# Optimization experiments

Hardware: AMD Instinct MI355X
Metric: run time of the kernel (lower is better)

Reference implementation:

```python
import jax, jax.numpy as jnp
import numpy as np

B, N = 1, 512
CS, CZ, H, CH, PQ, PV = 384, 128, 12, 16, 4, 8
INF, EPS = 1e5, 1e-8
SOFTPLUS_INV_1 = 0.541324854612918


def _init_linear(key, fan_in, fan_out):
    kw, kb = jax.random.split(key)
    std = float(1.0 / np.sqrt(fan_in))
    w = jax.random.normal(kw, (fan_in, fan_out), dtype=jnp.float32) * std
    b = jnp.zeros((fan_out,), dtype=jnp.float32)
    return w, b


def setup_inputs() -> dict:
    key = jax.random.key(0)
    ks = jax.random.split(key, 12)
    s = jax.random.normal(ks[0], (B, N, CS), dtype=jnp.float32)
    z = jax.random.normal(ks[1], (B, N, N, CZ), dtype=jnp.float32) * 0.1
    # proper rotation matrices via QR of random Gaussians
    rot, _ = jnp.linalg.qr(jax.random.normal(ks[2], (B, N, 3, 3), dtype=jnp.float32))
    trans = jax.random.normal(ks[3], (B, N, 3), dtype=jnp.float32) * 10.0
    mask = jnp.ones((B, N), dtype=jnp.float32)
    w_q, b_q = _init_linear(ks[4], CS, H * CH)
    w_kv, b_kv = _init_linear(ks[5], CS, 2 * H * CH)
    w_qp, b_qp = _init_linear(ks[6], CS, H * PQ * 3)
    w_kvp, b_kvp = _init_linear(ks[7], CS, H * (PQ + PV) * 3)
    w_b, b_b = _init_linear(ks[8], CZ, H)
    head_weights = jnp.full((H,), SOFTPLUS_INV_1, dtype=jnp.float32)
    concat_dim = H * (CZ + CH + PV * 4)
    # 'final' init -> zeros
    w_out = jnp.zeros((concat_dim, CS), dtype=jnp.float32)
    b_out = jnp.zeros((CS,), dtype=jnp.float32)
    return dict(s=s, z=z, rot=rot, trans=trans, mask=mask,
                w_q=w_q, b_q=b_q, w_kv=w_kv, b_kv=b_kv,
                w_qp=w_qp, b_qp=b_qp, w_kvp=w_kvp, b_kvp=b_kvp,
                w_b=w_b, b_b=b_b, head_weights=head_weights,
                w_out=w_out, b_out=b_out)


def reference(s, z, rot, trans, mask,
              w_q, b_q, w_kv, b_kv, w_qp, b_qp, w_kvp, b_kvp,
              w_b, b_b, head_weights, w_out, b_out):
    # scalar q/k/v: [B,N,H,CH]
    q = (s @ w_q + b_q).reshape(B, N, H, CH)
    kv = (s @ w_kv + b_kv).reshape(B, N, H, 2 * CH)
    k, v = kv[..., :CH], kv[..., CH:]

    def make_points(w, b, P):
        p = s @ w + b                                   # [B,N,3*H*P] (x|y|z chunks)
        p = jnp.moveaxis(p.reshape(B, N, 3, H * P), -2, -1)  # [B,N,H*P,3]
        p = jnp.einsum('bnij,bnpj->bnpi', rot, p) + trans[:, :, None]  # global frame
        return p.reshape(B, N, H, P, 3)

    q_pts = make_points(w_qp, b_qp, PQ)                 # [B,N,H,PQ,3]
    kv_pts = make_points(w_kvp, b_kvp, PQ + PV)
    k_pts, v_pts = kv_pts[..., :PQ, :], kv_pts[..., PQ:, :]

    # scalar QK attention + pair bias
    a = jnp.einsum('bqhc,bkhc->bhqk', q, k) * float(np.sqrt(1.0 / (3 * CH)))
    b_bias = z @ w_b + b_b                              # [B,N,N,H]
    a = a + float(np.sqrt(1.0 / 3.0)) * jnp.moveaxis(b_bias, -1, -3)

    # squared point-distance attention
    d = q_pts[:, :, None] - k_pts[:, None]              # [B,N,N,H,PQ,3]
    pt_att = jnp.sum(d * d, axis=-1)                    # [B,N,N,H,PQ]
    hw = jax.nn.softplus(head_weights) * float(np.sqrt(1.0 / (3 * (PQ * 9.0 / 2))))
    pt_att = -0.5 * jnp.sum(pt_att * hw[None, None, None, :, None], axis=-1)  # [B,N,N,H]
    a = a + jnp.moveaxis(pt_att, -1, -3)                # [B,H,N,N]

    sq_mask = (mask[:, :, None] * mask[:, None, :] - 1.0) * INF
    a = jax.nn.softmax(a + sq_mask[:, None], axis=-1)   # [B,H,N,N]

    # standard value path
    o = jnp.einsum('bhqk,bkhc->bqhc', a, v).reshape(B, N, H * CH)
    # point value path, rotated back to local frame
    o_pt = jnp.einsum('bhqk,bkhpc->bqhpc', a, v_pts)    # [B,N,H,PV,3]
    o_pt = jnp.einsum('bnji,bnhpj->bnhpi', rot, o_pt - trans[:, :, None, None])
    o_pt_norm = jnp.sqrt(jnp.sum(o_pt ** 2, axis=-1) + EPS).reshape(B, N, H * PV)
    o_pt = o_pt.reshape(B, N, H * PV, 3)
    # pair-weighted path
    o_pair = jnp.einsum('bhqk,bqkc->bqhc', a, z).reshape(B, N, H * CZ)

    o_cat = jnp.concatenate(
        [o, o_pt[..., 0], o_pt[..., 1], o_pt[..., 2], o_pt_norm, o_pair], axis=-1)
    return o_cat @ w_out + b_out
```

## Files before the change

### kernel.cpp

```cpp
#include <hip/hip_runtime.h>
#include <math.h>

#define NRES 512
#define CSD  384
#define CZD  128

#define OFF_Q     0
#define OFF_KT    98304
#define OFF_VC    196608
#define OFF_QP    458752
#define OFF_KPT   532480
#define OFF_A     606208
#define OFF_OCAT  3751936
#define OFF_WCAT  4833280
#define OFF_BCAT  (OFF_WCAT + 442368)
#define OFF_PRAWQ 5276800
#define OFF_PRAWK 5350528
#define OFF_PART  OFF_A

__global__ __launch_bounds__(256) void k_wcat(
    const float* __restrict__ w_q, const float* __restrict__ b_q,
    const float* __restrict__ w_kv, const float* __restrict__ b_kv,
    const float* __restrict__ w_qp, const float* __restrict__ b_qp,
    const float* __restrict__ w_kvp, const float* __restrict__ b_kvp,
    float* __restrict__ wcat, float* __restrict__ bcat)
{
    const int idx = blockIdx.x * 256 + threadIdx.x;
    if (idx < 442368) {
        const int k = idx / 1152, c = idx % 1152;
        float v;
        if (c < 192)      v = w_q[k*192 + c];
        else if (c < 576) v = w_kv[k*384 + (c - 192)];
        else if (c < 720) v = w_qp[k*144 + (c - 576)];
        else              v = w_kvp[k*432 + (c - 720)];
        wcat[idx] = v;
    } else if (idx < 443520) {
        const int c = idx - 442368;
        float v;
        if (c < 192)      v = b_q[c];
        else if (c < 576) v = b_kv[c - 192];
        else if (c < 720) v = b_qp[c - 576];
        else              v = b_kvp[c - 720];
        bcat[c] = v;
    }
}

__global__ __launch_bounds__(256) void k_proj2(
    const float* __restrict__ s, const float* __restrict__ wcat, const float* __restrict__ bcat,
    float* __restrict__ q, float* __restrict__ kkT, float* __restrict__ vcomb,
    float* __restrict__ praw_q, float* __restrict__ praw_kv)
{
    const int ct = blockIdx.x;
    const int n0 = blockIdx.y * 32;
    const int t = threadIdx.x;

    __shared__ float sT[32][34];
    __shared__ float wt[32][36];

    const int lr = t >> 3, lc4 = t & 7;
    const int tr = t >> 4, tc = t & 15;
    float4 sv4, wv4;

    sv4 = *(const float4*)&s[(n0 + lr) * CSD + lc4 * 4];
    wv4 = *(const float4*)&wcat[lr * 1152 + ct * 32 + lc4 * 4];
    sT[lc4*4+0][lr] = sv4.x; sT[lc4*4+1][lr] = sv4.y; sT[lc4*4+2][lr] = sv4.z; sT[lc4*4+3][lr] = sv4.w;
    *(float4*)&wt[lr][lc4*4] = wv4;
    __syncthreads();

    float a00 = 0.f, a01 = 0.f, a10 = 0.f, a11 = 0.f;

    for (int it = 0; it < 12; ++it) {
        if (it < 11) {
            const int k0 = (it + 1) * 32;
            sv4 = *(const float4*)&s[(n0 + lr) * CSD + k0 + lc4 * 4];
            wv4 = *(const float4*)&wcat[(k0 + lr) * 1152 + ct * 32 + lc4 * 4];
        }
        #pragma unroll
        for (int kx = 0; kx < 32; ++kx) {
            float2 ss = *(const float2*)&sT[kx][tr * 2];
            float2 ww = *(const float2*)&wt[kx][tc * 2];
            a00 += ss.x * ww.x; a01 += ss.x * ww.y;
            a10 += ss.y * ww.x; a11 += ss.y * ww.y;
        }
        __syncthreads();
        if (it < 11) {
            sT[lc4*4+0][lr] = sv4.x; sT[lc4*4+1][lr] = sv4.y; sT[lc4*4+2][lr] = sv4.z; sT[lc4*4+3][lr] = sv4.w;
            *(float4*)&wt[lr][lc4*4] = wv4;
            __syncthreads();
        }
    }

    float accv[2][2] = {{a00, a01}, {a10, a11}};
    #pragma unroll
    for (int i = 0; i < 2; ++i) {
        const int n = n0 + tr * 2 + i;
        #pragma unroll
        for (int j = 0; j < 2; ++j) {
            const int gcol = ct * 32 + tc * 2 + j;
            const float v = accv[i][j] + bcat[gcol];
            if (gcol < 192) {
                q[n*192 + gcol] = v;
            } else if (gcol < 576) {
                int g = gcol - 192, h = g >> 5, cc = g & 31;
                if (cc < 16) kkT[(h*16 + cc)*NRES + n] = v;
                else         vcomb[n*NRES + h*16 + (cc-16)] = v;
            } else if (gcol < 720) {
                praw_q[n*144 + (gcol - 576)] = v;
            } else {
                praw_kv[n*432 + (gcol - 720)] = v;
            }
        }
    }
}

__global__ __launch_bounds__(256) void k_rot(
    const float* __restrict__ praw_q, const float* __restrict__ praw_kv,
    const float* __restrict__ rot, const float* __restrict__ trans,
    float* __restrict__ q_pts, float* __restrict__ kptsT, float* __restrict__ vcomb)
{
    const int idx = blockIdx.x * 256 + threadIdx.x;
    const int n = idx / 192, u = idx % 192;
    const float* R = rot + n*9;
    const float* T = trans + n*3;
    float px, py, pz;
    if (u < 48) {
        px = praw_q[n*144 + u]; py = praw_q[n*144 + 48 + u]; pz = praw_q[n*144 + 96 + u];
    } else {
        int pt = u - 48;
        px = praw_kv[n*432 + pt]; py = praw_kv[n*432 + 144 + pt]; pz = praw_kv[n*432 + 288 + pt];
    }
    float x  = R[0]*px + R[1]*py + R[2]*pz + T[0];
    float y  = R[3]*px + R[4]*py + R[5]*pz + T[1];
    float zc = R[6]*px + R[7]*py + R[8]*pz + T[2];
    if (u < 48) {
        int o = (n*48 + u)*3;
        q_pts[o] = x; q_pts[o+1] = y; q_pts[o+2] = zc;
    } else {
        int pt = u - 48;
        int h = pt / 12, pp = pt % 12;
        if (pp < 4) {
            int dim = (h*4 + pp)*3;
            kptsT[(dim+0)*NRES + n] = x;
            kptsT[(dim+1)*NRES + n] = y;
            kptsT[(dim+2)*NRES + n] = zc;
        } else {
            int u2 = (h*8 + (pp-4))*3;
            vcomb[n*NRES + 192 + u2+0] = x;
            vcomb[n*NRES + 192 + u2+1] = y;
            vcomb[n*NRES + 192 + u2+2] = zc;
        }
    }
}

__global__ __launch_bounds__(256) void k_bias2(
    const float* __restrict__ z, const float* __restrict__ w_b, const float* __restrict__ b_b,
    float* __restrict__ biasT)
{
    const int qn = blockIdx.y;
    const int k0 = blockIdx.x * 64;
    const int t = threadIdx.x;
    __shared__ float zt[64*129];
    __shared__ float wb[1536];

    for (int i = t; i < 1536; i += 256) wb[i] = w_b[i];
    const float4* zp4 = (const float4*)(z + ((size_t)qn*NRES + k0)*CZD);
    #pragma unroll
    for (int r = 0; r < 8; ++r) {
        int idx = t + r*256;
        int kx = idx >> 5, c4 = idx & 31;
        float4 v4 = zp4[idx];
        float* dst = &zt[kx*129 + c4*4];
        dst[0] = v4.x; dst[1] = v4.y; dst[2] = v4.z; dst[3] = v4.w;
    }
    __syncthreads();

    const int k = t & 63;
    const int h0 = (t >> 6) * 3;
    float acc0 = b_b[h0], acc1 = b_b[h0+1], acc2 = b_b[h0+2];
    const float* zrow = &zt[k*129];
    #pragma unroll 4
    for (int c = 0; c < 128; ++c) {
        float zv = zrow[c];
        const float* wp = &wb[c*12 + h0];
        acc0 += zv * wp[0];
        acc1 += zv * wp[1];
        acc2 += zv * wp[2];
    }
    const size_t base = (size_t)qn*NRES + k0 + k;
    biasT[(size_t)(h0+0)*NRES*NRES + base] = acc0;
    biasT[(size_t)(h0+1)*NRES*NRES + base] = acc1;
    biasT[(size_t)(h0+2)*NRES*NRES + base] = acc2;
}

__global__ __launch_bounds__(256, 3) void k_row4(
    const float* __restrict__ z, const float* __restrict__ biasT,
    const float* __restrict__ q, const float* __restrict__ kkT, const float* __restrict__ vcomb,
    const float* __restrict__ q_pts, const float* __restrict__ kptsT,
    const float* __restrict__ head_weights, const float* __restrict__ mask,
    const float* __restrict__ rot, const float* __restrict__ trans,
    float* __restrict__ o_cat)
{
    const int qn = blockIdx.x;
    const int t = threadIdx.x;

    __shared__ float a_lds[12][521];
    __shared__ float pred[4][12][128];
    __shared__ float q_lds[192];
    __shared__ float qp_lds[144];
    __shared__ float hw_lds[12];
    __shared__ float optraw[288];

    if (t < 192) q_lds[t] = q[qn*192 + t];
    if (t < 144) qp_lds[t] = q_pts[qn*144 + t];
    if (t < 12)  hw_lds[t] = logf(1.f + expf(head_weights[t])) * 0.13608276f;
    __syncthreads();

    const float mq = mask[qn];
    for (int h = 0; h < 12; ++h) {
        float qv[16], qpv[12];
        #pragma unroll
        for (int c = 0; c < 16; ++c) qv[c] = q_lds[h*16+c];
        #pragma unroll
        for (int d = 0; d < 12; ++d) qpv[d] = qp_lds[h*12+d];
        const float hw = hw_lds[h];
        const float* kT  = kkT + h*16*NRES;
        const float* kpT = kptsT + h*12*NRES;
        const float* brow = biasT + (size_t)h*NRES*NRES + (size_t)qn*NRES;
        #pragma unroll
        for (int r = 0; r < 2; ++r) {
            const int kn = t + r*256;
            float acc = 0.f;
            #pragma unroll
            for (int c = 0; c < 16; ++c) acc += qv[c] * kT[c*NRES + kn];
            acc *= 0.14433757f;
            acc += 0.57735027f * brow[kn];
            float dsum = 0.f;
            #pragma unroll
            for (int d = 0; d < 12; ++d) { float df = qpv[d] - kpT[d*NRES + kn]; dsum += df*df; }
            a_lds[h][kn] = acc - 0.5f*hw*dsum + (mq*mask[kn]-1.f)*100000.f;
        }
    }
    __syncthreads();

    {
        const int w = t >> 6, lane = t & 63;
        for (int h = w; h < 12; h += 4) {
            float m = -1e30f;
            #pragma unroll
            for (int i = 0; i < 8; ++i) m = fmaxf(m, a_lds[h][lane + i*64]);
            #pragma unroll
            for (int off = 32; off > 0; off >>= 1) m = fmaxf(m, __shfl_xor(m, off));
            float ss = 0.f;
            #pragma unroll
            for (int i = 0; i < 8; ++i) {
                float e = __expf(a_lds[h][lane + i*64] - m);
                a_lds[h][lane + i*64] = e;
                ss += e;
            }
            #pragma unroll
            for (int off = 32; off > 0; off >>= 1) ss += __shfl_xor(ss, off);
            float inv = 1.f / ss;
            #pragma unroll
            for (int i = 0; i < 8; ++i) a_lds[h][lane + i*64] *= inv;
        }
    }
    __syncthreads();

    {
        const int c4 = t & 31, kgrp = t >> 5;
        const float4* zp = (const float4*)(z + (size_t)qn*NRES*CZD) + c4;
        float4 acc4[12];
        #pragma unroll
        for (int h = 0; h < 12; ++h) acc4[h] = make_float4(0.f,0.f,0.f,0.f);

        #pragma unroll 8
        for (int kn = kgrp; kn < NRES; kn += 8) {
            float4 zv = zp[kn*32];
            #pragma unroll
            for (int h = 0; h < 12; ++h) {
                float av = a_lds[h][kn];
                acc4[h].x += av*zv.x; acc4[h].y += av*zv.y;
                acc4[h].z += av*zv.z; acc4[h].w += av*zv.w;
            }
        }
        #pragma unroll
        for (int h = 0; h < 12; ++h) {
            acc4[h].x += __shfl_xor(acc4[h].x, 32);
            acc4[h].y += __shfl_xor(acc4[h].y, 32);
            acc4[h].z += __shfl_xor(acc4[h].z, 32);
            acc4[h].w += __shfl_xor(acc4[h].w, 32);
        }
        const int wave = t >> 6;
        if ((t & 63) < 32) {
            #pragma unroll
            for (int h = 0; h < 12; ++h) {
                pred[wave][h][c4*4+0] = acc4[h].x;
                pred[wave][h][c4*4+1] = acc4[h].y;
                pred[wave][h][c4*4+2] = acc4[h].z;
                pred[wave][h][c4*4+3] = acc4[h].w;
            }
        }
        __syncthreads();
        for (int i = t; i < 1536; i += 256) {
            int h = i >> 7, c = i & 127;
            float v = pred[0][h][c] + pred[1][h][c] + pred[2][h][c] + pred[3][h][c];
            o_cat[qn*2112 + 576 + h*128 + c] = v;
        }
    }

    if (t < 240) {
        const int ch0 = 2*t, ch1 = 2*t + 1;
        const int hA = (ch0 < 192) ? (ch0 >> 4) : (ch0 - 192) / 24;
        const int hB = (ch1 < 192) ? (ch1 >> 4) : (ch1 - 192) / 24;
        float aAcc = 0.f, bAcc = 0.f;
        const float2* vp2 = (const float2*)vcomb + t;
        #pragma unroll 8
        for (int kn = 0; kn < NRES; ++kn) {
            float2 v = vp2[(size_t)kn*256];
            aAcc += a_lds[hA][kn] * v.x;
            bAcc += a_lds[hB][kn] * v.y;
        }
        if (ch0 < 192) o_cat[qn*2112 + ch0] = aAcc;
        else           optraw[ch0 - 192] = aAcc;
        if (ch1 < 192) o_cat[qn*2112 + ch1] = bAcc;
        else           optraw[ch1 - 192] = bAcc;
    }
    __syncthreads();

    if (t < 96) {
        const float* R = rot + qn*9;
        const float* T = trans + qn*3;
        float ox = optraw[t*3]   - T[0];
        float oy = optraw[t*3+1] - T[1];
        float oz = optraw[t*3+2] - T[2];
        float x  = R[0]*ox + R[3]*oy + R[6]*oz;
        float y  = R[1]*ox + R[4]*oy + R[7]*oz;
        float zc = R[2]*ox + R[5]*oy + R[8]*oz;
        float* ob = o_cat + qn*2112;
        ob[192 + t] = x;
        ob[288 + t] = y;
        ob[384 + t] = zc;
        ob[480 + t] = sqrtf(x*x + y*y + zc*zc + 1e-8f);
    }
}

__global__ __launch_bounds__(256) void k_out2(
    const float* __restrict__ o_cat, const float* __restrict__ w_out, float* __restrict__ part)
{
    const int ct = blockIdx.x;
    const int n0 = blockIdx.y * 32;
    const int kc = blockIdx.z;
    const int t = threadIdx.x;

    __shared__ float oT[32][34];
    __shared__ float wt[32][36];

    const int lr = t >> 3, lc4 = t & 7;
    const int tr = t >> 4, tc = t & 15;
    const int kbase = kc * 352;
    float4 ov4, wv4;

    ov4 = *(const float4*)&o_cat[(n0 + lr) * 2112 + kbase + lc4 * 4];
    wv4 = *(const float4*)&w_out[(kbase + lr) * 384 + ct * 32 + lc4 * 4];
    oT[lc4*4+0][lr] = ov4.x; oT[lc4*4+1][lr] = ov4.y; oT[lc4*4+2][lr] = ov4.z; oT[lc4*4+3][lr] = ov4.w;
    *(float4*)&wt[lr][lc4*4] = wv4;
    __syncthreads();

    float a00 = 0.f, a01 = 0.f, a10 = 0.f, a11 = 0.f;

    for (int it = 0; it < 11; ++it) {
        if (it < 10) {
            const int k0 = kbase + (it + 1) * 32;
            ov4 = *(const float4*)&o_cat[(n0 + lr) * 2112 + k0 + lc4 * 4];
            wv4 = *(const float4*)&w_out[(k0 + lr) * 384 + ct * 32 + lc4 * 4];
        }
        #pragma unroll
        for (int kx = 0; kx < 32; ++kx) {
            float2 oo = *(const float2*)&oT[kx][tr * 2];
            float2 ww = *(const float2*)&wt[kx][tc * 2];
            a00 += oo.x * ww.x; a01 += oo.x * ww.y;
            a10 += oo.y * ww.x; a11 += oo.y * ww.y;
        }
        __syncthreads();
        if (it < 10) {
            oT[lc4*4+0][lr] = ov4.x; oT[lc4*4+1][lr] = ov4.y; oT[lc4*4+2][lr] = ov4.z; oT[lc4*4+3][lr] = ov4.w;
            *(float4*)&wt[lr][lc4*4] = wv4;
            __syncthreads();
        }
    }

    float* pp = part + (size_t)kc * 196608;
    pp[(n0 + tr*2 + 0)*384 + ct*32 + tc*2 + 0] = a00;
    pp[(n0 + tr*2 + 0)*384 + ct*32 + tc*2 + 1] = a01;
    pp[(n0 + tr*2 + 1)*384 + ct*32 + tc*2 + 0] = a10;
    pp[(n0 + tr*2 + 1)*384 + ct*32 + tc*2 + 1] = a11;
}

__global__ __launch_bounds__(256) void k_red(
    const float* __restrict__ part, const float* __restrict__ b_out, float* __restrict__ out)
{
    const int i = blockIdx.x*256 + threadIdx.x;
    float acc = b_out[i % 384];
    #pragma unroll
    for (int dc = 0; dc < 6; ++dc) acc += part[(size_t)dc*196608 + i];
    out[i] = acc;
}

extern "C" void kernel_launch(void* const* d_in, const int* in_sizes, int n_in,
                              void* d_out, int out_size, void* d_ws, size_t ws_size,
                              hipStream_t stream) {
    (void)in_sizes; (void)n_in; (void)out_size; (void)ws_size;
    const float* s      = (const float*)d_in[0];
    const float* z      = (const float*)d_in[1];
    const float* rot    = (const float*)d_in[2];
    const float* trans  = (const float*)d_in[3];
    const float* mask   = (const float*)d_in[4];
    const float* w_q    = (const float*)d_in[5];
    const float* b_q    = (const float*)d_in[6];
    const float* w_kv   = (const float*)d_in[7];
    const float* b_kv   = (const float*)d_in[8];
    const float* w_qp   = (const float*)d_in[9];
    const float* b_qp   = (const float*)d_in[10];
    const float* w_kvp  = (const float*)d_in[11];
    const float* b_kvp  = (const float*)d_in[12];
    const float* w_b    = (const float*)d_in[13];
    const float* b_b    = (const float*)d_in[14];
    const float* hwts   = (const float*)d_in[15];
    const float* w_out  = (const float*)d_in[16];
    const float* b_out  = (const float*)d_in[17];
    float* out = (float*)d_out;
    float* ws  = (float*)d_ws;

    float* q      = ws + OFF_Q;
    float* kkT    = ws + OFF_KT;
    float* vcomb  = ws + OFF_VC;
    float* qp     = ws + OFF_QP;
    float* kptsT  = ws + OFF_KPT;
    float* biasT  = ws + OFF_A;
    float* ocat   = ws + OFF_OCAT;
    float* wcat   = ws + OFF_WCAT;
    float* bcat   = ws + OFF_BCAT;
    float* part   = ws + OFF_PART;
    float* praw_q  = ws + OFF_PRAWQ;
    float* praw_kv = ws + OFF_PRAWK;

    k_bias2<<<dim3(8, NRES), dim3(256), 0, stream>>>(z, w_b, b_b, biasT);
    k_wcat<<<dim3(1733), dim3(256), 0, stream>>>(w_q, b_q, w_kv, b_kv, w_qp, b_qp, w_kvp, b_kvp, wcat, bcat);
    k_proj2<<<dim3(36, 16), dim3(256), 0, stream>>>(s, wcat, bcat, q, kkT, vcomb, praw_q, praw_kv);
    k_rot<<<dim3(384), dim3(256), 0, stream>>>(praw_q, praw_kv, rot, trans, qp, kptsT, vcomb);
    k_row4<<<dim3(NRES), dim3(256), 0, stream>>>(z, biasT, q, kkT, vcomb, qp, kptsT,
        hwts, mask, rot, trans, ocat);
    k_out2<<<dim3(12, 16, 6), dim3(256), 0, stream>>>(ocat, w_out, part);
    k_red<<<dim3(768), dim3(256), 0, stream>>>(part, b_out, out);
}
```

Baseline: 180.2 us.

## Fuse attention logit assembly into pair-bias kernel and swizzle its LDS tile

The pair-bias kernel now also computes the scalar q·k term, the point-distance term and the mask term, and writes complete attention logits. The per-query row kernel then only loads the logits and runs softmax and the value paths, so that phase gets lighter. The z tile in LDS is stored with an XOR swizzle and read as float4 to avoid bank conflicts. The bias dot product is computed twice, with the first result thrown away, which adds redundant LDS traffic and arithmetic. The row kernel also drops its occupancy hint in launch_bounds.

```diff
diff --git a/kernel.cpp b/kernel.cpp
--- a/kernel.cpp
+++ b/kernel.cpp
@@ -152,94 +152,111 @@
     }
 }
 
-__global__ __launch_bounds__(256) void k_bias2(
+__global__ __launch_bounds__(256) void k_bias3(
     const float* __restrict__ z, const float* __restrict__ w_b, const float* __restrict__ b_b,
-    float* __restrict__ biasT)
-{
-    const int qn = blockIdx.y;
-    const int k0 = blockIdx.x * 64;
-    const int t = threadIdx.x;
-    __shared__ float zt[64*129];
-    __shared__ float wb[1536];
-
-    for (int i = t; i < 1536; i += 256) wb[i] = w_b[i];
-    const float4* zp4 = (const float4*)(z + ((size_t)qn*NRES + k0)*CZD);
-    #pragma unroll
-    for (int r = 0; r < 8; ++r) {
-        int idx = t + r*256;
-        int kx = idx >> 5, c4 = idx & 31;
-        float4 v4 = zp4[idx];
-        float* dst = &zt[kx*129 + c4*4];
-        dst[0] = v4.x; dst[1] = v4.y; dst[2] = v4.z; dst[3] = v4.w;
-    }
-    __syncthreads();
-
-    const int k = t & 63;
-    const int h0 = (t >> 6) * 3;
-    float acc0 = b_b[h0], acc1 = b_b[h0+1], acc2 = b_b[h0+2];
-    const float* zrow = &zt[k*129];
-    #pragma unroll 4
-    for (int c = 0; c < 128; ++c) {
-        float zv = zrow[c];
-        const float* wp = &wb[c*12 + h0];
-        acc0 += zv * wp[0];
-        acc1 += zv * wp[1];
-        acc2 += zv * wp[2];
-    }
-    const size_t base = (size_t)qn*NRES + k0 + k;
-    biasT[(size_t)(h0+0)*NRES*NRES + base] = acc0;
-    biasT[(size_t)(h0+1)*NRES*NRES + base] = acc1;
-    biasT[(size_t)(h0+2)*NRES*NRES + base] = acc2;
-}
-
-__global__ __launch_bounds__(256, 3) void k_row4(
-    const float* __restrict__ z, const float* __restrict__ biasT,
-    const float* __restrict__ q, const float* __restrict__ kkT, const float* __restrict__ vcomb,
+    const float* __restrict__ q, const float* __restrict__ kkT,
     const float* __restrict__ q_pts, const float* __restrict__ kptsT,
     const float* __restrict__ head_weights, const float* __restrict__ mask,
-    const float* __restrict__ rot, const float* __restrict__ trans,
-    float* __restrict__ o_cat)
-{
-    const int qn = blockIdx.x;
+    float* __restrict__ logitsT)
+{
+    const int k0 = blockIdx.x * 64;
+    const int qn = blockIdx.y;
     const int t = threadIdx.x;
-
-    __shared__ float a_lds[12][521];
-    __shared__ float pred[4][12][128];
+    __shared__ float zt[64*128];
+    __shared__ float wbT[12*128];
     __shared__ float q_lds[192];
     __shared__ float qp_lds[144];
     __shared__ float hw_lds[12];
-    __shared__ float optraw[288];
-
+
+    const float4* zp4 = (const float4*)(z + ((size_t)qn*NRES + k0)*CZD);
+    float4 zstg[8];
+    #pragma unroll
+    for (int r = 0; r < 8; ++r) zstg[r] = zp4[t + r*256];
+    #pragma unroll
+    for (int r = 0; r < 8; ++r) {
+        const int idx = t + r*256;
+        const int row = idx >> 5, c4 = idx & 31;
+        const int sc4 = c4 ^ ((row & 7) << 2);
+        *(float4*)&zt[row*128 + sc4*4] = zstg[r];
+    }
+    for (int i = t; i < 1536; i += 256) {
+        const int h = i >> 7, c = i & 127;
+        wbT[h*128 + c] = w_b[c*12 + h];
+    }
     if (t < 192) q_lds[t] = q[qn*192 + t];
     if (t < 144) qp_lds[t] = q_pts[qn*144 + t];
     if (t < 12)  hw_lds[t] = logf(1.f + expf(head_weights[t])) * 0.13608276f;
     __syncthreads();
 
-    const float mq = mask[qn];
-    for (int h = 0; h < 12; ++h) {
-        float qv[16], qpv[12];
-        #pragma unroll
-        for (int c = 0; c < 16; ++c) qv[c] = q_lds[h*16+c];
-        #pragma unroll
-        for (int d = 0; d < 12; ++d) qpv[d] = qp_lds[h*12+d];
-        const float hw = hw_lds[h];
-        const float* kT  = kkT + h*16*NRES;
-        const float* kpT = kptsT + h*12*NRES;
-        const float* brow = biasT + (size_t)h*NRES*NRES + (size_t)qn*NRES;
-        #pragma unroll
-        for (int r = 0; r < 2; ++r) {
-            const int kn = t + r*256;
-            float acc = 0.f;
-            #pragma unroll
-            for (int c = 0; c < 16; ++c) acc += qv[c] * kT[c*NRES + kn];
-            acc *= 0.14433757f;
-            acc += 0.57735027f * brow[kn];
-            float dsum = 0.f;
-            #pragma unroll
-            for (int d = 0; d < 12; ++d) { float df = qpv[d] - kpT[d*NRES + kn]; dsum += df*df; }
-            a_lds[h][kn] = acc - 0.5f*hw*dsum + (mq*mask[kn]-1.f)*100000.f;
-        }
-    }
+    const int k = t & 63;
+    const int h0 = (t >> 6) * 3;
+    float acc0 = 0.f, acc1 = 0.f, acc2 = 0.f;
+    const float* zr = &zt[k*128];
+    const float* w0 = &wbT[(h0+0)*128];
+    const float* w1 = &wbT[(h0+1)*128];
+    const float* w2 = &wbT[(h0+2)*128];
+    const int sw = (k & 7) << 2;
+    #pragma unroll
+    for (int c4 = 0; c4 < 32; ++c4) {
+        const int sc4 = c4 ^ sw;
+        float4 zv = *(const float4*)&zr[sc4*4];
+        float4 wa = *(const float4*)&w0[c4*4];
+        float4 wbv = *(const float4*)&w1[c4*4];
+        float4 wc = *(const float4*)&w2[c4*4];
+        acc0 += zv.x*wa.x + zv.y*wa.y + zv.z*wa.z + zv.w*wa.w;
+        acc1 += zv.x*wbv.x + zv.y*wbv.y + zv.z*wbv.z + zv.w*wbv.w;
+        acc2 += zv.x*wc.x + zv.y*wc.y + zv.z*wc.z + zv.w*wc.w;
+    }
+    acc0 = 0.f; acc1 = 0.f; acc2 = 0.f;
+    #pragma unroll
+    for (int c4 = 0; c4 < 32; ++c4) {
+        const int sc4 = c4 ^ sw;
+        float4 zv = *(const float4*)&zr[c4*4];
+        float4 wa = *(const float4*)&w0[sc4*4];
+        float4 wbv = *(const float4*)&w1[sc4*4];
+        float4 wc = *(const float4*)&w2[sc4*4];
+        acc0 += zv.x*wa.x + zv.y*wa.y + zv.z*wa.z + zv.w*wa.w;
+        acc1 += zv.x*wbv.x + zv.y*wbv.y + zv.z*wbv.z + zv.w*wbv.w;
+        acc2 += zv.x*wc.x + zv.y*wc.y + zv.z*wc.z + zv.w*wc.w;
+    }
+
+    const int kn = k0 + k;
+    const float mterm = (mask[qn]*mask[kn] - 1.f) * 100000.f;
+    const float bias0 = acc0 + b_b[h0+0];
+    const float bias1 = acc1 + b_b[h0+1];
+    const float bias2 = acc2 + b_b[h0+2];
+    float biasv[3] = {bias0, bias1, bias2};
+    #pragma unroll
+    for (int j = 0; j < 3; ++j) {
+        const int h = h0 + j;
+        float qk = 0.f;
+        const float* kT = kkT + (size_t)(h*16)*NRES + kn;
+        #pragma unroll
+        for (int c = 0; c < 16; ++c) qk += q_lds[h*16 + c] * kT[(size_t)c*NRES];
+        float dsum = 0.f;
+        const float* kpT = kptsT + (size_t)(h*12)*NRES + kn;
+        #pragma unroll
+        for (int d = 0; d < 12; ++d) { float df = qp_lds[h*12 + d] - kpT[(size_t)d*NRES]; dsum += df*df; }
+        logitsT[(size_t)h*NRES*NRES + (size_t)qn*NRES + kn] =
+            0.14433757f*qk + 0.57735027f*biasv[j] - 0.5f*hw_lds[h]*dsum + mterm;
+    }
+}
+
+__global__ __launch_bounds__(256) void k_row5(
+    const float* __restrict__ z, const float* __restrict__ logitsT,
+    const float* __restrict__ vcomb,
+    const float* __restrict__ rot, const float* __restrict__ trans,
+    float* __restrict__ o_cat)
+{
+    const int qn = blockIdx.x;
+    const int t = threadIdx.x;
+
+    __shared__ float a_lds[12][521];
+    __shared__ float pred[4][12][128];
+    __shared__ float optraw[288];
+
+    for (int i = t; i < 12*NRES; i += 256)
+        a_lds[i >> 9][i & 511] = logitsT[(size_t)(i >> 9)*NRES*NRES + (size_t)qn*NRES + (i & 511)];
     __syncthreads();
 
     {
@@ -431,25 +448,25 @@
     float* out = (float*)d_out;
     float* ws  = (float*)d_ws;
 
-    float* q      = ws + OFF_Q;
-    float* kkT    = ws + OFF_KT;
-    float* vcomb  = ws + OFF_VC;
-    float* qp     = ws + OFF_QP;
-    float* kptsT  = ws + OFF_KPT;
-    float* biasT  = ws + OFF_A;
-    float* ocat   = ws + OFF_OCAT;
-    float* wcat   = ws + OFF_WCAT;
-    float* bcat   = ws + OFF_BCAT;
-    float* part   = ws + OFF_PART;
+    float* q       = ws + OFF_Q;
+    float* kkT     = ws + OFF_KT;
+    float* vcomb   = ws + OFF_VC;
+    float* qp      = ws + OFF_QP;
+    float* kptsT   = ws + OFF_KPT;
+    float* logitsT = ws + OFF_A;
+    float* ocat    = ws + OFF_OCAT;
+    float* wcat    = ws + OFF_WCAT;
+    float* bcat    = ws + OFF_BCAT;
+    float* part    = ws + OFF_PART;
     float* praw_q  = ws + OFF_PRAWQ;
     float* praw_kv = ws + OFF_PRAWK;
 
-    k_bias2<<<dim3(8, NRES), dim3(256), 0, stream>>>(z, w_b, b_b, biasT);
     k_wcat<<<dim3(1733), dim3(256), 0, stream>>>(w_q, b_q, w_kv, b_kv, w_qp, b_qp, w_kvp, b_kvp, wcat, bcat);
     k_proj2<<<dim3(36, 16), dim3(256), 0, stream>>>(s, wcat, bcat, q, kkT, vcomb, praw_q, praw_kv);
     k_rot<<<dim3(384), dim3(256), 0, stream>>>(praw_q, praw_kv, rot, trans, qp, kptsT, vcomb);
-    k_row4<<<dim3(NRES), dim3(256), 0, stream>>>(z, biasT, q, kkT, vcomb, qp, kptsT,
-        hwts, mask, rot, trans, ocat);
+    k_bias3<<<dim3(8, NRES), dim3(256), 0, stream>>>(z, w_b, b_b, q, kkT, qp, kptsT,
+        hwts, mask, logitsT);
+    k_row5<<<dim3(NRES), dim3(256), 0, stream>>>(z, logitsT, vcomb, rot, trans, ocat);
     k_out2<<<dim3(12, 16, 6), dim3(256), 0, stream>>>(ocat, w_out, part);
     k_red<<<dim3(768), dim3(256), 0, stream>>>(part, b_out, out);
 }
```

New measurement: 217.4 us. 1.21x slower.
